# Optimization experiments

Hardware: AMD Instinct MI355X
Metric: run time of the kernel (lower is better)

The kernel has to match this reference:

```python
import jax, jax.numpy as jnp
import numpy as np

N_NODES = 100000
N_EDGES = 1600000
NF = 64
EF = 32
BN_EPS = 1e-5


def setup_inputs() -> dict:
    key = jax.random.key(0)
    ks = jax.random.split(key, 12)
    node_feats = jax.random.normal(ks[0], (N_NODES, NF), dtype=jnp.float32)
    edge_feats = jax.random.normal(ks[1], (N_EDGES, EF), dtype=jnp.float32)
    src = jax.random.randint(ks[2], (N_EDGES,), 0, N_NODES, dtype=jnp.int32)
    dst = jax.random.randint(ks[3], (N_EDGES,), 0, N_NODES, dtype=jnp.int32)
    # Linear params stored as [in, out]; scaled like torch default init (1/sqrt(in)).
    def lin(k, fin, fout):
        k1, k2 = jax.random.split(k)
        bound = 1.0 / np.sqrt(fin)
        W = jax.random.uniform(k1, (fin, fout), jnp.float32, -bound, bound)
        b = jax.random.uniform(k2, (fout,), jnp.float32, -bound, bound)
        return W, b
    W_src, b_src = lin(ks[4], NF, 2 * NF)
    W_dst, b_dst = lin(ks[5], NF, 2 * NF)
    W_edge, b_edge = lin(ks[6], EF, 2 * NF)
    gamma_m = jnp.ones((2 * NF,), jnp.float32)
    beta_m = jnp.zeros((2 * NF,), jnp.float32)
    gamma_n = jnp.ones((NF,), jnp.float32)
    beta_n = jnp.zeros((NF,), jnp.float32)
    return {
        "node_feats": node_feats, "edge_feats": edge_feats,
        "W_src": W_src, "b_src": b_src,
        "W_dst": W_dst, "b_dst": b_dst,
        "W_edge": W_edge, "b_edge": b_edge,
        "gamma_m": gamma_m, "beta_m": beta_m,
        "gamma_n": gamma_n, "beta_n": beta_n,
        "src": src, "dst": dst,
    }


def _batchnorm(x, gamma, beta):
    # Training-mode batch norm with biased variance (as torch BatchNorm1d in train).
    mean = jnp.mean(x, axis=0)
    var = jnp.var(x, axis=0)
    return (x - mean) * (gamma * jax.lax.rsqrt(var + BN_EPS)) + beta


def reference(node_feats, edge_feats, W_src, b_src, W_dst, b_dst, W_edge, b_edge,
              gamma_m, beta_m, gamma_n, beta_n, src, dst):
    h_src = node_feats @ W_src + b_src            # [N, 2F]
    h_dst = node_feats @ W_dst + b_dst            # [N, 2F]
    # u_add_v edge gather + edge linear
    m = h_src[src] + h_dst[dst] + (edge_feats @ W_edge + b_edge)  # [E, 2F]
    m = _batchnorm(m, gamma_m, beta_m)
    h_f, h_s = m[:, :NF], m[:, NF:]
    m = jax.nn.sigmoid(h_f) * jax.nn.softplus(h_s)  # gated message [E, F]
    # scatter-sum messages to destination nodes
    h = jax.ops.segment_sum(m, dst, num_segments=N_NODES)  # [N, F]
    h = _batchnorm(h, gamma_n, beta_n)
    return jax.nn.softplus(node_feats + h)
```

## Files before the change

kernel.cpp:

```cpp
#include <hip/hip_runtime.h>
#include <hip/hip_bf16.h>
#include <stdint.h>

#define NNODES 100000
#define NEDGES 1600000
#define C2 128
#define EFEAT 32
#define BN_EPS 1e-5f
#define CH 32
#define SCAN_B ((NNODES + 255) / 256)

typedef __hip_bfloat16 bf16;

__device__ __forceinline__ float bflo(uint32_t u) { return __uint_as_float(u << 16); }
__device__ __forceinline__ float bfhi(uint32_t u) { return __uint_as_float(u & 0xffff0000u); }
__device__ __forceinline__ float sigm(float x) { return 1.0f / (1.0f + __expf(-x)); }
__device__ __forceinline__ float softp(float x) { return fmaxf(x, 0.0f) + __logf(1.0f + __expf(-fabsf(x))); }

struct TB {};
struct TF {};

template <class T> struct LD;
template <> struct LD<TB> {
    static __device__ __forceinline__ float ld(const void* p, size_t i) {
        return __bfloat162float(((const bf16*)p)[i]);
    }
    static __device__ __forceinline__ float2 ld2(const void* p, size_t i) {
        const uint32_t u = *(const uint32_t*)((const bf16*)p + i);
        return make_float2(bflo(u), bfhi(u));
    }
    static __device__ __forceinline__ float4 ld4(const void* p, size_t i) {
        const uint2 v = *(const uint2*)((const bf16*)p + i);
        return make_float4(bflo(v.x), bfhi(v.x), bflo(v.y), bfhi(v.y));
    }
    static __device__ __forceinline__ void st2(void* p, size_t i, float a, float b) {
        union { bf16 h[2]; uint32_t u; } pk;
        pk.h[0] = __float2bfloat16(a);
        pk.h[1] = __float2bfloat16(b);
        *(uint32_t*)((bf16*)p + i) = pk.u;
    }
};
template <> struct LD<TF> {
    static __device__ __forceinline__ float ld(const void* p, size_t i) {
        return ((const float*)p)[i];
    }
    static __device__ __forceinline__ float2 ld2(const void* p, size_t i) {
        return *(const float2*)((const float*)p + i);
    }
    static __device__ __forceinline__ float4 ld4(const void* p, size_t i) {
        return *(const float4*)((const float*)p + i);
    }
    static __device__ __forceinline__ void st2(void* p, size_t i, float a, float b) {
        *(float2*)((float*)p + i) = make_float2(a, b);
    }
};

__global__ void k_detect(const uint32_t* __restrict__ nodeb, int* __restrict__ flag) {
    __shared__ int sfp;
    if (threadIdx.x == 0) sfp = 0;
    __syncthreads();
    const float v = fabsf(bflo(nodeb[threadIdx.x]));
    if (v > 1e10f) sfp = 1;
    __syncthreads();
    if (threadIdx.x == 0) *flag = sfp;
}

__global__ __launch_bounds__(256) void k_hist(const int* __restrict__ dst,
                                              int* __restrict__ cnt) {
    for (int e = blockIdx.x * 256 + threadIdx.x; e < NEDGES; e += gridDim.x * 256)
        atomicAdd(&cnt[dst[e]], 1);
}

__global__ __launch_bounds__(256) void k_scan1(const int* __restrict__ cnt,
                                               int* __restrict__ bsum) {
    __shared__ int red[256];
    const int t = threadIdx.x;
    const int i = blockIdx.x * 256 + t;
    red[t] = (i < NNODES) ? cnt[i] : 0;
    __syncthreads();
    for (int s = 128; s > 0; s >>= 1) {
        if (t < s) red[t] += red[t + s];
        __syncthreads();
    }
    if (t == 0) bsum[blockIdx.x] = red[0];
}

__global__ void k_scan2(int* __restrict__ bsum) {
    __shared__ int sh[512];
    const int t = threadIdx.x;
    const int v0 = (t < SCAN_B) ? bsum[t] : 0;
    sh[t] = v0;
    __syncthreads();
    for (int ofs = 1; ofs < 512; ofs <<= 1) {
        const int v = (t >= ofs) ? sh[t - ofs] : 0;
        __syncthreads();
        sh[t] += v;
        __syncthreads();
    }
    if (t < SCAN_B) bsum[t] = sh[t] - v0;
}

__global__ __launch_bounds__(256) void k_scan3(const int* __restrict__ cnt,
                                               const int* __restrict__ bsum,
                                               int* __restrict__ off,
                                               int* __restrict__ cur) {
    __shared__ int sh[256];
    const int t = threadIdx.x;
    const int i = blockIdx.x * 256 + t;
    const int orig = (i < NNODES) ? cnt[i] : 0;
    sh[t] = orig;
    __syncthreads();
    for (int ofs = 1; ofs < 256; ofs <<= 1) {
        const int v = (t >= ofs) ? sh[t - ofs] : 0;
        __syncthreads();
        sh[t] += v;
        __syncthreads();
    }
    const int excl = sh[t] - orig + bsum[blockIdx.x];
    if (i < NNODES) { off[i] = excl; cur[i] = excl; }
    if (i == NNODES) off[NNODES] = excl;
}

__global__ __launch_bounds__(256) void k_fill(const int* __restrict__ dst,
                                              int* __restrict__ cur,
                                              int* __restrict__ eid) {
    for (int e = blockIdx.x * 256 + threadIdx.x; e < NEDGES; e += gridDim.x * 256) {
        const int p = atomicAdd(&cur[dst[e]], 1);
        eid[p] = e;
    }
}

template <class T>
__device__ __forceinline__ void tables_body(
    const void* node, const void* Wsrc, const void* bsrc,
    const void* Wdst, const void* bdst, bf16* tsrc, bf16* tdst, float* x)
{
    const int t = threadIdx.x;
    const int col = t & 127;
    const void* W = (t < 128) ? Wsrc : Wdst;
    float w[64];
#pragma unroll
    for (int k = 0; k < 64; ++k) w[k] = LD<T>::ld(W, k * C2 + col);
    const float b = (t < 128) ? LD<T>::ld(bsrc, col) : LD<T>::ld(bdst, col);
    bf16* tab = (t < 128) ? tsrc : tdst;
    const int pos = (col < 64) ? (2 * col) : (2 * col - 127);
    for (int base = blockIdx.x * 4; base < NNODES; base += gridDim.x * 4) {
        x[t] = LD<T>::ld(node, (size_t)base * 64 + t);
        __syncthreads();
        float a0 = b, a1 = b, a2 = b, a3 = b;
#pragma unroll
        for (int k = 0; k < 64; ++k) {
            const float wv = w[k];
            a0 = fmaf(x[k], wv, a0);
            a1 = fmaf(x[64 + k], wv, a1);
            a2 = fmaf(x[128 + k], wv, a2);
            a3 = fmaf(x[192 + k], wv, a3);
        }
        __syncthreads();
        tab[(size_t)(base + 0) * C2 + pos] = __float2bfloat16(a0);
        tab[(size_t)(base + 1) * C2 + pos] = __float2bfloat16(a1);
        tab[(size_t)(base + 2) * C2 + pos] = __float2bfloat16(a2);
        tab[(size_t)(base + 3) * C2 + pos] = __float2bfloat16(a3);
    }
}

__global__ __launch_bounds__(256, 4) void k_tables(
    const void* node, const void* Wsrc, const void* bsrc,
    const void* Wdst, const void* bdst, bf16* tsrc, bf16* tdst, const int* flag)
{
    __shared__ float x[256];
    if (*flag) tables_body<TF>(node, Wsrc, bsrc, Wdst, bdst, tsrc, tdst, x);
    else       tables_body<TB>(node, Wsrc, bsrc, Wdst, bdst, tsrc, tdst, x);
}

template <class T>
__device__ __forceinline__ void edge_stats_body(
    const void* ef, const int* src, const int* dst, const void* We, const void* be,
    const uint32_t* tsrc, const uint32_t* tdst, float* mstats,
    float* efb, int* sidx, int* didx, float* red)
{
    const int t = threadIdx.x;
    const int c = t & 63;
    const int eg = t >> 6;
    float w0[EFEAT], w1[EFEAT];
#pragma unroll
    for (int k = 0; k < EFEAT; ++k) {
        w0[k] = LD<T>::ld(We, k * C2 + c);
        w1[k] = LD<T>::ld(We, k * C2 + c + 64);
    }
    const float be0 = LD<T>::ld(be, c), be1 = LD<T>::ld(be, c + 64);
    float s0 = 0.f, q0 = 0.f, s1 = 0.f, q1 = 0.f;
    for (int chunk = blockIdx.x * CH; chunk < NEDGES; chunk += gridDim.x * CH) {
        ((float4*)efb)[t] = LD<T>::ld4(ef, (size_t)chunk * EFEAT + 4 * t);
        if (t < CH) sidx[t] = src[chunk + t];
        else if (t < 2 * CH) didx[t - CH] = dst[chunk + t - CH];
        __syncthreads();
        for (int e0 = 0; e0 < CH; e0 += 4) {
            const int e = e0 + eg;
            const int s = sidx[e], d = didx[e];
            float el0 = be0, el1 = be1;
            const float4* efv = (const float4*)(efb + e * EFEAT);
#pragma unroll
            for (int k4 = 0; k4 < EFEAT / 4; ++k4) {
                const float4 f = efv[k4];
                el0 = fmaf(f.x, w0[4 * k4 + 0], el0); el1 = fmaf(f.x, w1[4 * k4 + 0], el1);
                el0 = fmaf(f.y, w0[4 * k4 + 1], el0); el1 = fmaf(f.y, w1[4 * k4 + 1], el1);
                el0 = fmaf(f.z, w0[4 * k4 + 2], el0); el1 = fmaf(f.z, w1[4 * k4 + 2], el1);
                el0 = fmaf(f.w, w0[4 * k4 + 3], el0); el1 = fmaf(f.w, w1[4 * k4 + 3], el1);
            }
            const uint32_t us = tsrc[(size_t)s * 64 + c];
            const uint32_t ud = tdst[(size_t)d * 64 + c];
            const float m0 = el0 + bflo(us) + bflo(ud);
            const float m1 = el1 + bfhi(us) + bfhi(ud);
            s0 += m0; q0 += m0 * m0;
            s1 += m1; q1 += m1 * m1;
        }
        __syncthreads();
    }
    ((float4*)red)[t] = make_float4(s0, q0, s1, q1);
    __syncthreads();
    if (t < 64) {
        float a0 = 0.f, a1 = 0.f, a2 = 0.f, a3 = 0.f;
        for (int g = 0; g < 4; ++g) {
            const float4 r = ((const float4*)red)[g * 64 + t];
            a0 += r.x; a1 += r.y; a2 += r.z; a3 += r.w;
        }
        atomicAdd(&mstats[t], a0);
        atomicAdd(&mstats[C2 + t], a1);
        atomicAdd(&mstats[t + 64], a2);
        atomicAdd(&mstats[C2 + t + 64], a3);
    }
}

__global__ __launch_bounds__(256, 4) void k_edge_stats(
    const void* ef, const int* src, const int* dst, const void* We, const void* be,
    const uint32_t* tsrc, const uint32_t* tdst, float* mstats, const int* flag)
{
    __shared__ float efb[CH * EFEAT];
    __shared__ int sidx[CH], didx[CH];
    __shared__ float red[1024];
    if (*flag) edge_stats_body<TF>(ef, src, dst, We, be, tsrc, tdst, mstats, efb, sidx, didx, red);
    else       edge_stats_body<TB>(ef, src, dst, We, be, tsrc, tdst, mstats, efb, sidx, didx, red);
}

template <class T>
__device__ __forceinline__ void fin_m_body(const float* mstats, const void* gamma,
                                           const void* beta, float* mss)
{
    const int c = threadIdx.x;
    const float inv = 1.0f / (float)NEDGES;
    const float mean = mstats[c] * inv;
    const float var = fmaxf(mstats[C2 + c] * inv - mean * mean, 0.0f);
    const float sc = LD<T>::ld(gamma, c) * rsqrtf(var + BN_EPS);
    mss[c] = sc;
    mss[C2 + c] = LD<T>::ld(beta, c) - mean * sc;
}

__global__ void k_fin_m(const float* mstats, const void* gamma, const void* beta,
                        float* mss, const int* flag)
{
    if (*flag) fin_m_body<TF>(mstats, gamma, beta, mss);
    else       fin_m_body<TB>(mstats, gamma, beta, mss);
}

#define EFMA(W0v, W1v, fv)                                        \
    el0 = fmaf((fv).x, (W0v).x, el0); el1 = fmaf((fv).x, (W1v).x, el1); \
    el0 = fmaf((fv).y, (W0v).y, el0); el1 = fmaf((fv).y, (W1v).y, el1); \
    el0 = fmaf((fv).z, (W0v).z, el0); el1 = fmaf((fv).z, (W1v).z, el1); \
    el0 = fmaf((fv).w, (W0v).w, el0); el1 = fmaf((fv).w, (W1v).w, el1);

#define LDW(j)                                                                       \
    const float4 W0##j = make_float4(LD<T>::ld(We, (4 * j + 0) * C2 + c),            \
                                     LD<T>::ld(We, (4 * j + 1) * C2 + c),            \
                                     LD<T>::ld(We, (4 * j + 2) * C2 + c),            \
                                     LD<T>::ld(We, (4 * j + 3) * C2 + c));           \
    const float4 W1##j = make_float4(LD<T>::ld(We, (4 * j + 0) * C2 + c + 64),       \
                                     LD<T>::ld(We, (4 * j + 1) * C2 + c + 64),       \
                                     LD<T>::ld(We, (4 * j + 2) * C2 + c + 64),       \
                                     LD<T>::ld(We, (4 * j + 3) * C2 + c + 64));

template <class T>
__device__ __forceinline__ void aggregate_body(
    const void* ef, const int* src, const void* We, const void* be,
    const uint32_t* tsrc, const uint32_t* tdst, const float* mss,
    const int* off, const int* eid, float* hacc, float* nstats, float* red)
{
    const int t = threadIdx.x;
    const int c = t & 63;
    const int g = t >> 6;
    LDW(0) LDW(1) LDW(2) LDW(3) LDW(4) LDW(5) LDW(6) LDW(7)
    const float be0 = LD<T>::ld(be, c), be1 = LD<T>::ld(be, c + 64);
    const float sc0 = mss[c], sh0 = mss[C2 + c];
    const float sc1 = mss[c + 64], sh1 = mss[C2 + c + 64];
    float s = 0.f, q = 0.f;
    for (int d0 = blockIdx.x * 4; d0 < NNODES; d0 += gridDim.x * 4) {
        const int d = d0 + g;
        const uint32_t ud = tdst[(size_t)d * 64 + c];
        const float hd0 = bflo(ud), hd1 = bfhi(ud);
        const int beg = __builtin_amdgcn_readfirstlane(off[d]);
        const int end = __builtin_amdgcn_readfirstlane(off[d + 1]);
        float acc = 0.f;
        for (int b = beg; b < end; b += 64) {
            const int nb = min(64, end - b);
            const int eb = (b + c < end) ? eid[b + c] : 0;
            const int sb = (b + c < end) ? src[eb] : 0;
            for (int i = 0; i < nb; ++i) {
                const int e = __shfl(eb, i, 64);
                const int sn = __shfl(sb, i, 64);
                const uint32_t us = tsrc[(size_t)sn * 64 + c];
                const size_t eb4 = (size_t)e * EFEAT;
                const float4 f0 = LD<T>::ld4(ef, eb4 + 0);
                const float4 f1 = LD<T>::ld4(ef, eb4 + 4);
                const float4 f2 = LD<T>::ld4(ef, eb4 + 8);
                const float4 f3 = LD<T>::ld4(ef, eb4 + 12);
                const float4 f4 = LD<T>::ld4(ef, eb4 + 16);
                const float4 f5 = LD<T>::ld4(ef, eb4 + 20);
                const float4 f6 = LD<T>::ld4(ef, eb4 + 24);
                const float4 f7 = LD<T>::ld4(ef, eb4 + 28);
                float el0 = be0, el1 = be1;
                EFMA(W00, W10, f0) EFMA(W01, W11, f1)
                EFMA(W02, W12, f2) EFMA(W03, W13, f3)
                EFMA(W04, W14, f4) EFMA(W05, W15, f5)
                EFMA(W06, W16, f6) EFMA(W07, W17, f7)
                const float m0 = el0 + bflo(us) + hd0;
                const float m1 = el1 + bfhi(us) + hd1;
                acc += sigm(fmaf(m0, sc0, sh0)) * softp(fmaf(m1, sc1, sh1));
            }
        }
        hacc[(size_t)d * 64 + c] = acc;
        s += acc; q += acc * acc;
    }
    red[t] = s; red[256 + t] = q;
    __syncthreads();
    if (t < 64) {
        float a = 0.f, b = 0.f;
        for (int gg = 0; gg < 4; ++gg) { a += red[gg * 64 + t]; b += red[256 + gg * 64 + t]; }
        atomicAdd(&nstats[t], a);
        atomicAdd(&nstats[64 + t], b);
    }
}

__global__ __launch_bounds__(256, 4) void k_aggregate(
    const void* ef, const int* src, const void* We, const void* be,
    const uint32_t* tsrc, const uint32_t* tdst, const float* mss,
    const int* off, const int* eid, float* hacc, float* nstats, const int* flag)
{
    __shared__ float red[512];
    if (*flag) aggregate_body<TF>(ef, src, We, be, tsrc, tdst, mss, off, eid, hacc, nstats, red);
    else       aggregate_body<TB>(ef, src, We, be, tsrc, tdst, mss, off, eid, hacc, nstats, red);
}

template <class T>
__device__ __forceinline__ void fin_n_body(const float* nstats, const void* gamma,
                                           const void* beta, float* nss)
{
    const int c = threadIdx.x;
    const float inv = 1.0f / (float)NNODES;
    const float mean = nstats[c] * inv;
    const float var = fmaxf(nstats[64 + c] * inv - mean * mean, 0.0f);
    const float sc = LD<T>::ld(gamma, c) * rsqrtf(var + BN_EPS);
    nss[c] = sc;
    nss[64 + c] = LD<T>::ld(beta, c) - mean * sc;
}

__global__ void k_fin_n(const float* nstats, const void* gamma, const void* beta,
                        float* nss, const int* flag)
{
    if (*flag) fin_n_body<TF>(nstats, gamma, beta, nss);
    else       fin_n_body<TB>(nstats, gamma, beta, nss);
}

template <class T>
__device__ __forceinline__ void out_body(const void* node, const float* hacc,
                                         const float* nss, void* out)
{
    const int t = threadIdx.x;
    const int64_t npairs = (int64_t)NNODES * 32;
    int64_t i = (int64_t)blockIdx.x * 256 + t;
    const int c0 = (int)((i * 2) & 63);
    const float sc0 = nss[c0], sh0 = nss[64 + c0];
    const float sc1 = nss[c0 + 1], sh1 = nss[64 + c0 + 1];
    const float2* hp = (const float2*)hacc;
    const int64_t stride = (int64_t)gridDim.x * 256;
    for (; i < npairs; i += stride) {
        const float2 nv = LD<T>::ld2(node, (size_t)(2 * i));
        const float2 h = hp[i];
        const float v0 = softp(nv.x + fmaf(h.x, sc0, sh0));
        const float v1 = softp(nv.y + fmaf(h.y, sc1, sh1));
        LD<T>::st2(out, (size_t)(2 * i), v0, v1);
    }
}

__global__ __launch_bounds__(256) void k_out(const void* node, const float* hacc,
                                             const float* nss, void* out, const int* flag)
{
    if (*flag) out_body<TF>(node, hacc, nss, out);
    else       out_body<TB>(node, hacc, nss, out);
}

extern "C" void kernel_launch(void* const* d_in, const int* in_sizes, int n_in,
                              void* d_out, int out_size, void* d_ws, size_t ws_size,
                              hipStream_t stream)
{
    const void* node = d_in[0];
    const void* ef   = d_in[1];
    const void* Wsrc = d_in[2];
    const void* bsrc = d_in[3];
    const void* Wdst = d_in[4];
    const void* bdst = d_in[5];
    const void* We   = d_in[6];
    const void* be   = d_in[7];
    const void* gm   = d_in[8];
    const void* bm   = d_in[9];
    const void* gn   = d_in[10];
    const void* bn   = d_in[11];
    const int* src   = (const int*)d_in[12];
    const int* dst   = (const int*)d_in[13];

    float* hacc   = (float*)d_ws;
    float* mstats = hacc + (size_t)NNODES * 64;
    float* nstats = mstats + 256;
    float* mss    = nstats + 128;
    float* nss    = mss + 256;
    int* flag     = (int*)(nss + 128);
    bf16* tsrc    = (bf16*)(flag + 4);
    bf16* tdst    = tsrc + (size_t)NNODES * C2;
    int* cnt      = (int*)(tdst + (size_t)NNODES * C2);
    int* off      = cnt + NNODES;
    int* cur      = off + NNODES + 1;
    int* bsum     = cur + NNODES;
    int* eid      = bsum + 512;

    hipMemsetAsync(mstats, 0, 384 * sizeof(float), stream);
    hipMemsetAsync(cnt, 0, NNODES * sizeof(int), stream);
    k_detect<<<1, 256, 0, stream>>>((const uint32_t*)node, flag);
    k_hist<<<2048, 256, 0, stream>>>(dst, cnt);
    k_scan1<<<SCAN_B, 256, 0, stream>>>(cnt, bsum);
    k_scan2<<<1, 512, 0, stream>>>(bsum);
    k_scan3<<<SCAN_B, 256, 0, stream>>>(cnt, bsum, off, cur);
    k_fill<<<2048, 256, 0, stream>>>(dst, cur, eid);
    k_tables<<<512, 256, 0, stream>>>(node, Wsrc, bsrc, Wdst, bdst, tsrc, tdst, flag);
    k_edge_stats<<<2048, 256, 0, stream>>>(ef, src, dst, We, be,
                                           (const uint32_t*)tsrc, (const uint32_t*)tdst,
                                           mstats, flag);
    k_fin_m<<<1, 128, 0, stream>>>(mstats, gm, bm, mss, flag);
    k_aggregate<<<2048, 256, 0, stream>>>(ef, src, We, be,
                                          (const uint32_t*)tsrc, (const uint32_t*)tdst,
                                          mss, off, eid, hacc, nstats, flag);
    k_fin_n<<<1, 64, 0, stream>>>(nstats, gn, bn, nss, flag);
    k_out<<<1024, 256, 0, stream>>>(node, hacc, nss, d_out, flag);
}
```

Before: 1.258 ms.

## Permute edge features and src into dst-sorted order during CSR fill

The fill kernel now writes src indices and edge-feature rows (packed to bf16) into dst-sorted order, removing the eid indirection. The separate edge-stats kernel is replaced by a templated edge pass that walks the CSR layout and reads contiguous feature rows, with one-edge-ahead prefetching of the next row and src-table entry. This cuts random gathers of edge features in both passes. The cost is a larger scatter write in fill, and the fp32 path now rounds edge features to bf16.

New measurement: 1.209 ms. 1.04x faster.

```diff
diff --git a/kernel.cpp b/kernel.cpp
--- a/kernel.cpp
+++ b/kernel.cpp
@@ -7,7 +7,6 @@
 #define C2 128
 #define EFEAT 32
 #define BN_EPS 1e-5f
-#define CH 32
 #define SCAN_B ((NNODES + 255) / 256)
 
 typedef __hip_bfloat16 bf16;
@@ -16,6 +15,12 @@
 __device__ __forceinline__ float bfhi(uint32_t u) { return __uint_as_float(u & 0xffff0000u); }
 __device__ __forceinline__ float sigm(float x) { return 1.0f / (1.0f + __expf(-x)); }
 __device__ __forceinline__ float softp(float x) { return fmaxf(x, 0.0f) + __logf(1.0f + __expf(-fabsf(x))); }
+__device__ __forceinline__ uint32_t pk2(float a, float b) {
+    union { bf16 h[2]; uint32_t u; } pk;
+    pk.h[0] = __float2bfloat16(a);
+    pk.h[1] = __float2bfloat16(b);
+    return pk.u;
+}
 
 struct TB {};
 struct TF {};
@@ -29,15 +34,12 @@
         const uint32_t u = *(const uint32_t*)((const bf16*)p + i);
         return make_float2(bflo(u), bfhi(u));
     }
-    static __device__ __forceinline__ float4 ld4(const void* p, size_t i) {
-        const uint2 v = *(const uint2*)((const bf16*)p + i);
-        return make_float4(bflo(v.x), bfhi(v.x), bflo(v.y), bfhi(v.y));
-    }
     static __device__ __forceinline__ void st2(void* p, size_t i, float a, float b) {
-        union { bf16 h[2]; uint32_t u; } pk;
-        pk.h[0] = __float2bfloat16(a);
-        pk.h[1] = __float2bfloat16(b);
-        *(uint32_t*)((bf16*)p + i) = pk.u;
+        *(uint32_t*)((bf16*)p + i) = pk2(a, b);
+    }
+    static __device__ __forceinline__ void ldrow(const void* p, size_t e, uint4* o) {
+        const uint4* er = (const uint4*)p + e * 4;
+        o[0] = er[0]; o[1] = er[1]; o[2] = er[2]; o[3] = er[3];
     }
 };
 template <> struct LD<TF> {
@@ -47,11 +49,16 @@
     static __device__ __forceinline__ float2 ld2(const void* p, size_t i) {
         return *(const float2*)((const float*)p + i);
     }
-    static __device__ __forceinline__ float4 ld4(const void* p, size_t i) {
-        return *(const float4*)((const float*)p + i);
-    }
     static __device__ __forceinline__ void st2(void* p, size_t i, float a, float b) {
         *(float2*)((float*)p + i) = make_float2(a, b);
+    }
+    static __device__ __forceinline__ void ldrow(const void* p, size_t e, uint4* o) {
+        const float4* fr = (const float4*)p + e * 8;
+#pragma unroll
+        for (int j = 0; j < 4; ++j) {
+            const float4 a = fr[2 * j], b = fr[2 * j + 1];
+            o[j] = make_uint4(pk2(a.x, a.y), pk2(a.z, a.w), pk2(b.x, b.y), pk2(b.z, b.w));
+        }
     }
 };
 
@@ -121,13 +128,34 @@
     if (i == NNODES) off[NNODES] = excl;
 }
 
+template <class T>
+__device__ __forceinline__ void fill_body(const int* __restrict__ dst,
+                                          const int* __restrict__ src,
+                                          const void* __restrict__ ef,
+                                          int* __restrict__ cur,
+                                          int* __restrict__ srcp,
+                                          uint4* __restrict__ efp4)
+{
+    for (int e = blockIdx.x * 256 + threadIdx.x; e < NEDGES; e += gridDim.x * 256) {
+        uint4 o[4];
+        LD<T>::ldrow(ef, e, o);
+        const int p = atomicAdd(&cur[dst[e]], 1);
+        srcp[p] = src[e];
+        uint4* w = efp4 + (size_t)p * 4;
+        w[0] = o[0]; w[1] = o[1]; w[2] = o[2]; w[3] = o[3];
+    }
+}
+
 __global__ __launch_bounds__(256) void k_fill(const int* __restrict__ dst,
+                                              const int* __restrict__ src,
+                                              const void* __restrict__ ef,
                                               int* __restrict__ cur,
-                                              int* __restrict__ eid) {
-    for (int e = blockIdx.x * 256 + threadIdx.x; e < NEDGES; e += gridDim.x * 256) {
-        const int p = atomicAdd(&cur[dst[e]], 1);
-        eid[p] = e;
-    }
+                                              int* __restrict__ srcp,
+                                              uint4* __restrict__ efp4,
+                                              const int* __restrict__ flag)
+{
+    if (*flag) fill_body<TF>(dst, src, ef, cur, srcp, efp4);
+    else       fill_body<TB>(dst, src, ef, cur, srcp, efp4);
 }
 
 template <class T>
@@ -174,76 +202,6 @@
 }
 
 template <class T>
-__device__ __forceinline__ void edge_stats_body(
-    const void* ef, const int* src, const int* dst, const void* We, const void* be,
-    const uint32_t* tsrc, const uint32_t* tdst, float* mstats,
-    float* efb, int* sidx, int* didx, float* red)
-{
-    const int t = threadIdx.x;
-    const int c = t & 63;
-    const int eg = t >> 6;
-    float w0[EFEAT], w1[EFEAT];
-#pragma unroll
-    for (int k = 0; k < EFEAT; ++k) {
-        w0[k] = LD<T>::ld(We, k * C2 + c);
-        w1[k] = LD<T>::ld(We, k * C2 + c + 64);
-    }
-    const float be0 = LD<T>::ld(be, c), be1 = LD<T>::ld(be, c + 64);
-    float s0 = 0.f, q0 = 0.f, s1 = 0.f, q1 = 0.f;
-    for (int chunk = blockIdx.x * CH; chunk < NEDGES; chunk += gridDim.x * CH) {
-        ((float4*)efb)[t] = LD<T>::ld4(ef, (size_t)chunk * EFEAT + 4 * t);
-        if (t < CH) sidx[t] = src[chunk + t];
-        else if (t < 2 * CH) didx[t - CH] = dst[chunk + t - CH];
-        __syncthreads();
-        for (int e0 = 0; e0 < CH; e0 += 4) {
-            const int e = e0 + eg;
-            const int s = sidx[e], d = didx[e];
-            float el0 = be0, el1 = be1;
-            const float4* efv = (const float4*)(efb + e * EFEAT);
-#pragma unroll
-            for (int k4 = 0; k4 < EFEAT / 4; ++k4) {
-                const float4 f = efv[k4];
-                el0 = fmaf(f.x, w0[4 * k4 + 0], el0); el1 = fmaf(f.x, w1[4 * k4 + 0], el1);
-                el0 = fmaf(f.y, w0[4 * k4 + 1], el0); el1 = fmaf(f.y, w1[4 * k4 + 1], el1);
-                el0 = fmaf(f.z, w0[4 * k4 + 2], el0); el1 = fmaf(f.z, w1[4 * k4 + 2], el1);
-                el0 = fmaf(f.w, w0[4 * k4 + 3], el0); el1 = fmaf(f.w, w1[4 * k4 + 3], el1);
-            }
-            const uint32_t us = tsrc[(size_t)s * 64 + c];
-            const uint32_t ud = tdst[(size_t)d * 64 + c];
-            const float m0 = el0 + bflo(us) + bflo(ud);
-            const float m1 = el1 + bfhi(us) + bfhi(ud);
-            s0 += m0; q0 += m0 * m0;
-            s1 += m1; q1 += m1 * m1;
-        }
-        __syncthreads();
-    }
-    ((float4*)red)[t] = make_float4(s0, q0, s1, q1);
-    __syncthreads();
-    if (t < 64) {
-        float a0 = 0.f, a1 = 0.f, a2 = 0.f, a3 = 0.f;
-        for (int g = 0; g < 4; ++g) {
-            const float4 r = ((const float4*)red)[g * 64 + t];
-            a0 += r.x; a1 += r.y; a2 += r.z; a3 += r.w;
-        }
-        atomicAdd(&mstats[t], a0);
-        atomicAdd(&mstats[C2 + t], a1);
-        atomicAdd(&mstats[t + 64], a2);
-        atomicAdd(&mstats[C2 + t + 64], a3);
-    }
-}
-
-__global__ __launch_bounds__(256, 4) void k_edge_stats(
-    const void* ef, const int* src, const int* dst, const void* We, const void* be,
-    const uint32_t* tsrc, const uint32_t* tdst, float* mstats, const int* flag)
-{
-    __shared__ float efb[CH * EFEAT];
-    __shared__ int sidx[CH], didx[CH];
-    __shared__ float red[1024];
-    if (*flag) edge_stats_body<TF>(ef, src, dst, We, be, tsrc, tdst, mstats, efb, sidx, didx, red);
-    else       edge_stats_body<TB>(ef, src, dst, We, be, tsrc, tdst, mstats, efb, sidx, didx, red);
-}
-
-template <class T>
 __device__ __forceinline__ void fin_m_body(const float* mstats, const void* gamma,
                                            const void* beta, float* mss)
 {
@@ -263,11 +221,13 @@
     else       fin_m_body<TB>(mstats, gamma, beta, mss);
 }
 
-#define EFMA(W0v, W1v, fv)                                        \
-    el0 = fmaf((fv).x, (W0v).x, el0); el1 = fmaf((fv).x, (W1v).x, el1); \
-    el0 = fmaf((fv).y, (W0v).y, el0); el1 = fmaf((fv).y, (W1v).y, el1); \
-    el0 = fmaf((fv).z, (W0v).z, el0); el1 = fmaf((fv).z, (W1v).z, el1); \
-    el0 = fmaf((fv).w, (W0v).w, el0); el1 = fmaf((fv).w, (W1v).w, el1);
+#define EFMAD(ua, ub, W0v, W1v) {                                   \
+    const float fx = bflo(ua), fy = bfhi(ua);                       \
+    const float fz = bflo(ub), fw = bfhi(ub);                       \
+    el0 = fmaf(fx, (W0v).x, el0); el1 = fmaf(fx, (W1v).x, el1);     \
+    el0 = fmaf(fy, (W0v).y, el0); el1 = fmaf(fy, (W1v).y, el1);     \
+    el0 = fmaf(fz, (W0v).z, el0); el1 = fmaf(fz, (W1v).z, el1);     \
+    el0 = fmaf(fw, (W0v).w, el0); el1 = fmaf(fw, (W1v).w, el1); }
 
 #define LDW(j)                                                                       \
     const float4 W0##j = make_float4(LD<T>::ld(We, (4 * j + 0) * C2 + c),            \
@@ -279,20 +239,25 @@
                                      LD<T>::ld(We, (4 * j + 2) * C2 + c + 64),       \
                                      LD<T>::ld(We, (4 * j + 3) * C2 + c + 64));
 
-template <class T>
-__device__ __forceinline__ void aggregate_body(
-    const void* ef, const int* src, const void* We, const void* be,
-    const uint32_t* tsrc, const uint32_t* tdst, const float* mss,
-    const int* off, const int* eid, float* hacc, float* nstats, float* red)
+template <class T, bool STATS>
+__device__ __forceinline__ void edge_pass_body(
+    const uint4* __restrict__ efp4, const int* __restrict__ srcp,
+    const void* __restrict__ We, const void* __restrict__ be,
+    const uint32_t* __restrict__ tsrc, const uint32_t* __restrict__ tdst,
+    const float* __restrict__ mss, const int* __restrict__ off,
+    float* __restrict__ hacc, float* __restrict__ ost, float* __restrict__ red)
 {
     const int t = threadIdx.x;
     const int c = t & 63;
     const int g = t >> 6;
     LDW(0) LDW(1) LDW(2) LDW(3) LDW(4) LDW(5) LDW(6) LDW(7)
     const float be0 = LD<T>::ld(be, c), be1 = LD<T>::ld(be, c + 64);
-    const float sc0 = mss[c], sh0 = mss[C2 + c];
-    const float sc1 = mss[c + 64], sh1 = mss[C2 + c + 64];
-    float s = 0.f, q = 0.f;
+    float sc0 = 0.f, sh0 = 0.f, sc1 = 0.f, sh1 = 0.f;
+    if constexpr (!STATS) {
+        sc0 = mss[c];      sh0 = mss[C2 + c];
+        sc1 = mss[c + 64]; sh1 = mss[C2 + c + 64];
+    }
+    float s0 = 0.f, q0 = 0.f, s1 = 0.f, q1 = 0.f;
     for (int d0 = blockIdx.x * 4; d0 < NNODES; d0 += gridDim.x * 4) {
         const int d = d0 + g;
         const uint32_t ud = tdst[(size_t)d * 64 + c];
@@ -302,52 +267,82 @@
         float acc = 0.f;
         for (int b = beg; b < end; b += 64) {
             const int nb = min(64, end - b);
-            const int eb = (b + c < end) ? eid[b + c] : 0;
-            const int sb = (b + c < end) ? src[eb] : 0;
+            const int sb = (b + c < end) ? srcp[b + c] : 0;
+            uint4 n0, n1, n2, n3;
+            {
+                const uint4* rp = efp4 + (size_t)b * 4;
+                n0 = rp[0]; n1 = rp[1]; n2 = rp[2]; n3 = rp[3];
+            }
+            uint32_t usn = tsrc[(size_t)__shfl(sb, 0, 64) * 64 + c];
             for (int i = 0; i < nb; ++i) {
-                const int e = __shfl(eb, i, 64);
-                const int sn = __shfl(sb, i, 64);
-                const uint32_t us = tsrc[(size_t)sn * 64 + c];
-                const size_t eb4 = (size_t)e * EFEAT;
-                const float4 f0 = LD<T>::ld4(ef, eb4 + 0);
-                const float4 f1 = LD<T>::ld4(ef, eb4 + 4);
-                const float4 f2 = LD<T>::ld4(ef, eb4 + 8);
-                const float4 f3 = LD<T>::ld4(ef, eb4 + 12);
-                const float4 f4 = LD<T>::ld4(ef, eb4 + 16);
-                const float4 f5 = LD<T>::ld4(ef, eb4 + 20);
-                const float4 f6 = LD<T>::ld4(ef, eb4 + 24);
-                const float4 f7 = LD<T>::ld4(ef, eb4 + 28);
+                const uint4 r0 = n0, r1 = n1, r2 = n2, r3 = n3;
+                const uint32_t us = usn;
+                if (i + 1 < nb) {
+                    const uint4* rp = efp4 + (size_t)(b + i + 1) * 4;
+                    n0 = rp[0]; n1 = rp[1]; n2 = rp[2]; n3 = rp[3];
+                    usn = tsrc[(size_t)__shfl(sb, i + 1, 64) * 64 + c];
+                }
                 float el0 = be0, el1 = be1;
-                EFMA(W00, W10, f0) EFMA(W01, W11, f1)
-                EFMA(W02, W12, f2) EFMA(W03, W13, f3)
-                EFMA(W04, W14, f4) EFMA(W05, W15, f5)
-                EFMA(W06, W16, f6) EFMA(W07, W17, f7)
+                EFMAD(r0.x, r0.y, W00, W10) EFMAD(r0.z, r0.w, W01, W11)
+                EFMAD(r1.x, r1.y, W02, W12) EFMAD(r1.z, r1.w, W03, W13)
+                EFMAD(r2.x, r2.y, W04, W14) EFMAD(r2.z, r2.w, W05, W15)
+                EFMAD(r3.x, r3.y, W06, W16) EFMAD(r3.z, r3.w, W07, W17)
                 const float m0 = el0 + bflo(us) + hd0;
                 const float m1 = el1 + bfhi(us) + hd1;
-                acc += sigm(fmaf(m0, sc0, sh0)) * softp(fmaf(m1, sc1, sh1));
+                if constexpr (STATS) {
+                    s0 += m0; q0 += m0 * m0;
+                    s1 += m1; q1 += m1 * m1;
+                } else {
+                    acc += sigm(fmaf(m0, sc0, sh0)) * softp(fmaf(m1, sc1, sh1));
+                }
             }
         }
-        hacc[(size_t)d * 64 + c] = acc;
-        s += acc; q += acc * acc;
-    }
-    red[t] = s; red[256 + t] = q;
-    __syncthreads();
-    if (t < 64) {
-        float a = 0.f, b = 0.f;
-        for (int gg = 0; gg < 4; ++gg) { a += red[gg * 64 + t]; b += red[256 + gg * 64 + t]; }
-        atomicAdd(&nstats[t], a);
-        atomicAdd(&nstats[64 + t], b);
-    }
-}
-
-__global__ __launch_bounds__(256, 4) void k_aggregate(
-    const void* ef, const int* src, const void* We, const void* be,
-    const uint32_t* tsrc, const uint32_t* tdst, const float* mss,
-    const int* off, const int* eid, float* hacc, float* nstats, const int* flag)
-{
-    __shared__ float red[512];
-    if (*flag) aggregate_body<TF>(ef, src, We, be, tsrc, tdst, mss, off, eid, hacc, nstats, red);
-    else       aggregate_body<TB>(ef, src, We, be, tsrc, tdst, mss, off, eid, hacc, nstats, red);
+        if constexpr (!STATS) {
+            hacc[(size_t)d * 64 + c] = acc;
+            s0 += acc; q0 += acc * acc;
+        }
+    }
+    if constexpr (STATS) {
+        ((float4*)red)[t] = make_float4(s0, q0, s1, q1);
+        __syncthreads();
+        if (t < 64) {
+            float a0 = 0.f, a1 = 0.f, a2 = 0.f, a3 = 0.f;
+            for (int gg = 0; gg < 4; ++gg) {
+                const float4 r = ((const float4*)red)[gg * 64 + t];
+                a0 += r.x; a1 += r.y; a2 += r.z; a3 += r.w;
+            }
+            atomicAdd(&ost[t], a0);
+            atomicAdd(&ost[C2 + t], a1);
+            atomicAdd(&ost[t + 64], a2);
+            atomicAdd(&ost[C2 + t + 64], a3);
+        }
+    } else {
+        red[t] = s0; red[256 + t] = q0;
+        __syncthreads();
+        if (t < 64) {
+            float a = 0.f, b2 = 0.f;
+            for (int gg = 0; gg < 4; ++gg) {
+                a += red[gg * 64 + t];
+                b2 += red[256 + gg * 64 + t];
+            }
+            atomicAdd(&ost[t], a);
+            atomicAdd(&ost[64 + t], b2);
+        }
+    }
+}
+
+template <bool STATS>
+__global__ __attribute__((amdgpu_waves_per_eu(4, 4))) __launch_bounds__(256)
+void k_edge_pass(
+    const uint4* __restrict__ efp4, const int* __restrict__ srcp,
+    const void* __restrict__ We, const void* __restrict__ be,
+    const uint32_t* __restrict__ tsrc, const uint32_t* __restrict__ tdst,
+    const float* __restrict__ mss, const int* __restrict__ off,
+    float* __restrict__ hacc, float* __restrict__ ost, const int* __restrict__ flag)
+{
+    __shared__ float red[1024];
+    if (*flag) edge_pass_body<TF, STATS>(efp4, srcp, We, be, tsrc, tdst, mss, off, hacc, ost, red);
+    else       edge_pass_body<TB, STATS>(efp4, srcp, We, be, tsrc, tdst, mss, off, hacc, ost, red);
 }
 
 template <class T>
@@ -429,7 +424,8 @@
     int* off      = cnt + NNODES;
     int* cur      = off + NNODES + 1;
     int* bsum     = cur + NNODES;
-    int* eid      = bsum + 512;
+    int* srcp     = bsum + 512;
+    bf16* efp     = (bf16*)((((uintptr_t)(srcp + NEDGES)) + 15) & ~(uintptr_t)15);
 
     hipMemsetAsync(mstats, 0, 384 * sizeof(float), stream);
     hipMemsetAsync(cnt, 0, NNODES * sizeof(int), stream);
@@ -438,15 +434,17 @@
     k_scan1<<<SCAN_B, 256, 0, stream>>>(cnt, bsum);
     k_scan2<<<1, 512, 0, stream>>>(bsum);
     k_scan3<<<SCAN_B, 256, 0, stream>>>(cnt, bsum, off, cur);
-    k_fill<<<2048, 256, 0, stream>>>(dst, cur, eid);
+    k_fill<<<2048, 256, 0, stream>>>(dst, src, ef, cur, srcp, (uint4*)efp, flag);
     k_tables<<<512, 256, 0, stream>>>(node, Wsrc, bsrc, Wdst, bdst, tsrc, tdst, flag);
-    k_edge_stats<<<2048, 256, 0, stream>>>(ef, src, dst, We, be,
-                                           (const uint32_t*)tsrc, (const uint32_t*)tdst,
-                                           mstats, flag);
+    k_edge_pass<true><<<2048, 256, 0, stream>>>(
+        (const uint4*)efp, srcp, We, be,
+        (const uint32_t*)tsrc, (const uint32_t*)tdst,
+        mss, off, hacc, mstats, flag);
     k_fin_m<<<1, 128, 0, stream>>>(mstats, gm, bm, mss, flag);
-    k_aggregate<<<2048, 256, 0, stream>>>(ef, src, We, be,
-                                          (const uint32_t*)tsrc, (const uint32_t*)tdst,
-                                          mss, off, eid, hacc, nstats, flag);
+    k_edge_pass<false><<<2048, 256, 0, stream>>>(
+        (const uint4*)efp, srcp, We, be,
+        (const uint32_t*)tsrc, (const uint32_t*)tdst,
+        mss, off, hacc, nstats, flag);
     k_fin_n<<<1, 64, 0, stream>>>(nstats, gn, bn, nss, flag);
     k_out<<<1024, 256, 0, stream>>>(node, hacc, nss, d_out, flag);
 }
```
